# Kernel optimization log

Hardware: AMD Instinct MI355X
Metric: run time of the kernel (lower is better)

Reference implementation:

```python
import jax, jax.numpy as jnp
import numpy as np

D = 1024      # model_dim
H = 2048      # expert hidden_dim
E = 8         # num routed experts
S = 1         # num shared experts
M = 4         # num modes (1 shared expert per mode)
TOP_K = 2
B, L = 2, 2048


def _ffn(x, w1, b1, w2, b2):
    # x: [T, D]; w1: [..., D, H]; stacked experts via einsum
    h = jnp.einsum('td,edh->teh', x, w1) + b1          # [T, E*, H]
    h = jax.nn.gelu(h)
    return jnp.einsum('teh,ehd->ted', h, w2) + b2      # [T, E*, D]


def setup_inputs() -> dict:
    key = jax.random.key(0)
    ks = jax.random.split(key, 16)
    s = 0.02
    inp = {
        'hidden': jax.random.normal(ks[0], (B, L, D), dtype=jnp.float32),
        'mode_ids': jax.random.randint(ks[1], (B, L), 0, M),
        'router_w': jax.random.normal(ks[2], (D, E), dtype=jnp.float32) * s,
        'router_b': jnp.zeros((E,), dtype=jnp.float32),
        'shared_w1': jax.random.normal(ks[3], (S, D, H), dtype=jnp.float32) * s,
        'shared_b1': jnp.zeros((S, H), dtype=jnp.float32),
        'shared_w2': jax.random.normal(ks[4], (S, H, D), dtype=jnp.float32) * s,
        'shared_b2': jnp.zeros((S, D), dtype=jnp.float32),
        'mode_w1': jax.random.normal(ks[5], (M, D, H), dtype=jnp.float32) * s,
        'mode_b1': jnp.zeros((M, H), dtype=jnp.float32),
        'mode_w2': jax.random.normal(ks[6], (M, H, D), dtype=jnp.float32) * s,
        'mode_b2': jnp.zeros((M, D), dtype=jnp.float32),
        'routed_w1': jax.random.normal(ks[7], (E, D, H), dtype=jnp.float32) * s,
        'routed_b1': jnp.zeros((E, H), dtype=jnp.float32),
        'routed_w2': jax.random.normal(ks[8], (E, H, D), dtype=jnp.float32) * s,
        'routed_b2': jnp.zeros((E, D), dtype=jnp.float32),
    }
    return inp


def reference(hidden, mode_ids, router_w, router_b,
              shared_w1, shared_b1, shared_w2, shared_b2,
              mode_w1, mode_b1, mode_w2, mode_b2,
              routed_w1, routed_b1, routed_w2, routed_b2):
    b, l, d = hidden.shape
    flat = hidden.reshape(b * l, d)                         # [T, D]

    # --- router ---
    router_logits = flat @ router_w + router_b              # [T, E]
    router_probs = jax.nn.softmax(router_logits, axis=-1)
    topk_probs, topk_indices = jax.lax.top_k(router_probs, TOP_K)  # [T, K]

    # --- shared experts (mean over S experts) ---
    shared_out = _ffn(flat, shared_w1, shared_b1, shared_w2, shared_b2).mean(axis=1)  # [T, D]

    # --- mode-conditioned shared experts (1 expert per mode) ---
    mode_flat = mode_ids.reshape(-1)                        # [T]
    mode_onehot = jax.nn.one_hot(mode_flat, M, dtype=flat.dtype)   # [T, M]
    mode_all = _ffn(flat, mode_w1, mode_b1, mode_w2, mode_b2)      # [T, M, D]
    mode_out = jnp.einsum('tm,tmd->td', mode_onehot, mode_all)
    shared_out = shared_out + mode_out

    # --- routed experts: combine weights per (token, expert) ---
    # w[t,e] = sum_k topk_probs[t,k] * (topk_indices[t,k] == e)
    combine_w = jnp.einsum('tke,tk->te',
                           jax.nn.one_hot(topk_indices, E, dtype=flat.dtype),
                           topk_probs)                      # [T, E]
    routed_all = _ffn(flat, routed_w1, routed_b1, routed_w2, routed_b2)  # [T, E, D]
    mixed = jnp.einsum('te,ted->td', combine_w, routed_all)

    output = (shared_out + mixed).reshape(b, l, d)
    aux_logits = router_logits.reshape(b, l, E)
    aux_idx = topk_indices.reshape(b, l, TOP_K)
    aux_probs = topk_probs.reshape(b, l, TOP_K)
    return output, aux_logits, aux_idx, aux_probs
```

## Files before the change

### kernel.cpp

```cpp
#include <hip/hip_runtime.h>
#include <hip/hip_bf16.h>

typedef __hip_bfloat16 bf16t;
using f32x4 = __attribute__((ext_vector_type(4))) float;
using s16x8 = __attribute__((ext_vector_type(8))) short;

#define NTOK 4096
#define DIM 1024
#define HID 2048
#define NEXP 8
#define NMODE 4
#define NGRP 13
#define SLOTS_PAD 16640
#define MAXT 144

static constexpr size_t SZ_WT    = (size_t)NGRP * HID * DIM * 2;
static constexpr size_t OFF_WT1  = 0;
static constexpr size_t OFF_OBUF = 0;
static constexpr size_t OFF_WT2  = OFF_WT1 + SZ_WT;
static constexpr size_t OFF_HBUF = OFF_WT2 + SZ_WT;
static constexpr size_t SZ_HBUF  = (size_t)SLOTS_PAD * HID * 2;
static constexpr size_t OFF_XBF  = OFF_HBUF + SZ_HBUF;
static constexpr size_t SZ_XBF   = (size_t)NTOK * DIM * 2;
static constexpr size_t OFF_B1   = OFF_XBF + SZ_XBF;
static constexpr size_t OFF_B2   = OFF_B1 + (size_t)NGRP * HID * 4;
static constexpr size_t OFF_TP   = OFF_B2 + (size_t)NGRP * DIM * 4;
static constexpr size_t OFF_TI   = OFF_TP + (size_t)NTOK * 2 * 4;
static constexpr size_t OFF_MS   = OFF_TI + (size_t)NTOK * 2 * 4;
static constexpr size_t OFF_R0S  = OFF_MS + (size_t)NTOK * 4;
static constexpr size_t OFF_R1S  = OFF_R0S + (size_t)NTOK * 4;
static constexpr size_t OFF_LIST = OFF_R1S + (size_t)NTOK * 4;
static constexpr size_t OFF_CNT  = OFF_LIST + (size_t)SLOTS_PAD * 4;
static constexpr size_t OFF_CUR  = OFF_CNT + 64;
static constexpr size_t OFF_TC   = OFF_CUR + 64;
static constexpr size_t OFF_TD   = OFF_TC + 16;
static constexpr size_t WS_NEED  = OFF_TD + (size_t)MAXT * 16;

static __device__ __forceinline__ short fb(float f) {
    bf16t h = __float2bfloat16(f);
    short s; __builtin_memcpy(&s, &h, 2); return s;
}
static __device__ __forceinline__ float bf2f(short s) {
    unsigned u = ((unsigned)(unsigned short)s) << 16;
    float f; __builtin_memcpy(&f, &u, 4); return f;
}

static __device__ __forceinline__ float fast_exp(float x) {
#if __has_builtin(__builtin_amdgcn_exp2f)
    return __builtin_amdgcn_exp2f(x * 1.4426950408889634f);
#else
    return exp2f(x * 1.4426950408889634f);
#endif
}
static __device__ __forceinline__ float fast_rcp(float x) {
#if __has_builtin(__builtin_amdgcn_rcpf)
    return __builtin_amdgcn_rcpf(x);
#else
    return 1.0f / x;
#endif
}
static __device__ __forceinline__ float gelu_tanh(float x) {
    float x2 = x * x;
    float u = 0.7978845608028654f * fmaf(0.044715f * x2, x, x);
    u = fminf(u, 15.0f);
    float t = fast_exp(2.0f * u);
    return x * t * fast_rcp(t + 1.0f);
}

typedef __attribute__((address_space(3))) void lds_void;
typedef const __attribute__((address_space(1))) void gbl_void;
static __device__ __forceinline__ void gload16(const void* g, void* l) {
    __builtin_amdgcn_global_load_lds((gbl_void*)g, (lds_void*)l, 16, 0, 0);
}

__global__ void router_k(const float* __restrict__ hidden, const int* __restrict__ mode_ids,
                         const float* __restrict__ rw, const float* __restrict__ rb,
                         float* __restrict__ aux_logits, float* __restrict__ aux_idx,
                         float* __restrict__ aux_probs,
                         float* __restrict__ topk_p, int* __restrict__ topk_i,
                         bf16t* __restrict__ xbf) {
    const int t = blockIdx.x;
    const int lane = threadIdx.x;
    const float* x = hidden + (size_t)t * DIM;
    float acc[NEXP];
#pragma unroll
    for (int e = 0; e < NEXP; e++) acc[e] = 0.f;
#pragma unroll
    for (int i = 0; i < DIM / 64; i++) {
        int d = i * 64 + lane;
        float xv = x[d];
        xbf[(size_t)t * DIM + d] = __float2bfloat16(xv);
        const float4* w = (const float4*)(rw + (size_t)d * NEXP);
        float4 w0 = w[0], w1 = w[1];
        acc[0] += xv * w0.x; acc[1] += xv * w0.y; acc[2] += xv * w0.z; acc[3] += xv * w0.w;
        acc[4] += xv * w1.x; acc[5] += xv * w1.y; acc[6] += xv * w1.z; acc[7] += xv * w1.w;
    }
#pragma unroll
    for (int off = 32; off >= 1; off >>= 1) {
#pragma unroll
        for (int e = 0; e < NEXP; e++) acc[e] += __shfl_down(acc[e], off, 64);
    }
    if (lane == 0) {
        float lg[NEXP], pb[NEXP];
        float mx = -1e30f;
#pragma unroll
        for (int e = 0; e < NEXP; e++) { lg[e] = acc[e] + rb[e]; mx = fmaxf(mx, lg[e]); }
        float s = 0.f;
#pragma unroll
        for (int e = 0; e < NEXP; e++) { pb[e] = expf(lg[e] - mx); s += pb[e]; }
        float inv = 1.f / s;
#pragma unroll
        for (int e = 0; e < NEXP; e++) { pb[e] *= inv; aux_logits[(size_t)t * NEXP + e] = lg[e]; }
        int i1 = 0;
        for (int e = 1; e < NEXP; e++) if (pb[e] > pb[i1]) i1 = e;
        int i2 = (i1 == 0) ? 1 : 0;
        for (int e = 0; e < NEXP; e++) { if (e == i1) continue; if (pb[e] > pb[i2]) i2 = e; }
        aux_idx[t * 2] = (float)i1;  aux_idx[t * 2 + 1] = (float)i2;
        aux_probs[t * 2] = pb[i1];   aux_probs[t * 2 + 1] = pb[i2];
        topk_p[t * 2] = pb[i1];      topk_p[t * 2 + 1] = pb[i2];
        topk_i[t * 2] = i1;          topk_i[t * 2 + 1] = i2;
    }
}

__global__ void count_k(const int* __restrict__ mode_ids, const int* __restrict__ topki,
                        int* __restrict__ cnts) {
    const int lane = threadIdx.x & 63;
    const int wave = threadIdx.x >> 6;
    int local[12];
#pragma unroll
    for (int i = 0; i < 12; i++) local[i] = 0;
    for (int c = wave; c < NTOK / 64; c += 4) {
        const int t = c * 64 + lane;
        const int m  = mode_ids[t];
        const int e0 = topki[t * 2];
        const int e1 = topki[t * 2 + 1];
#pragma unroll
        for (int b = 0; b < 4; b++) {
            unsigned long long k = __ballot(m == b);
            local[b] += __popcll(k);
        }
#pragma unroll
        for (int b = 0; b < 8; b++) {
            local[4 + b] += __popcll(__ballot(e0 == b));
            local[4 + b] += __popcll(__ballot(e1 == b));
        }
    }
    if (lane == 0) {
#pragma unroll
        for (int i = 0; i < 12; i++) atomicAdd(&cnts[i], local[i]);
    }
}

struct TPtr {
    const float* s_w1; const float* s_w2;
    const float* m_w1; const float* m_w2;
    const float* r_w1; const float* r_w2;
};
__global__ void transpose_convert_k(TPtr tp, bf16t* __restrict__ wt1, bf16t* __restrict__ wt2) {
    const size_t MSZ = (size_t)DIM * HID;
    int z = blockIdx.z;
    const float* src; bf16t* dst; int R, C;
    if (z == 0)      { src = tp.s_w1;                    dst = wt1;                 R = DIM; C = HID; }
    else if (z == 1) { src = tp.s_w2;                    dst = wt2;                 R = HID; C = DIM; }
    else if (z < 6)  { int m = z - 2;  src = tp.m_w1 + (size_t)m * MSZ; dst = wt1 + (size_t)(1 + m) * MSZ; R = DIM; C = HID; }
    else if (z < 10) { int m = z - 6;  src = tp.m_w2 + (size_t)m * MSZ; dst = wt2 + (size_t)(1 + m) * MSZ; R = HID; C = DIM; }
    else if (z < 18) { int e = z - 10; src = tp.r_w1 + (size_t)e * MSZ; dst = wt1 + (size_t)(5 + e) * MSZ; R = DIM; C = HID; }
    else             { int e = z - 18; src = tp.r_w2 + (size_t)e * MSZ; dst = wt2 + (size_t)(5 + e) * MSZ; R = HID; C = DIM; }
    int c0 = blockIdx.x * 64, r0 = blockIdx.y * 64;
    if (c0 >= C || r0 >= R) return;
    __shared__ float lds[64][65];
    const int t = threadIdx.x;
    const int ar = t >> 4, ac = (t & 15) * 4;
#pragma unroll
    for (int p = 0; p < 4; p++) {
        const int r = p * 16 + ar;
        const float4 v = *(const float4*)(src + (size_t)(r0 + r) * C + (c0 + ac));
        lds[r][ac] = v.x; lds[r][ac + 1] = v.y; lds[r][ac + 2] = v.z; lds[r][ac + 3] = v.w;
    }
    __syncthreads();
    const int bc = t >> 3;
    const int rg = (t & 7) * 8;
#pragma unroll
    for (int j = 0; j < 2; j++) {
        const int c = j * 32 + bc;
        unsigned w[4];
#pragma unroll
        for (int u = 0; u < 4; u++) {
            unsigned lo = (unsigned short)fb(lds[rg + 2 * u][c]);
            unsigned hi = (unsigned short)fb(lds[rg + 2 * u + 1][c]);
            w[u] = (hi << 16) | lo;
        }
        *(uint4*)((char*)dst + ((size_t)(c0 + c) * R + (r0 + rg)) * 2) = make_uint4(w[0], w[1], w[2], w[3]);
    }
}

__global__ void biascat_k(const float* __restrict__ sb1, const float* __restrict__ mb1, const float* __restrict__ rb1,
                          const float* __restrict__ sb2, const float* __restrict__ mb2, const float* __restrict__ rb2,
                          float* __restrict__ B1c, float* __restrict__ B2c) {
    int i = blockIdx.x * 256 + threadIdx.x;
    if (i < NGRP * HID) {
        int g = i / HID, h = i % HID;
        B1c[i] = (g == 0) ? sb1[h] : (g < 5) ? mb1[(g - 1) * HID + h] : rb1[(g - 5) * HID + h];
    }
    if (i < NGRP * DIM) {
        int g = i / DIM, d = i % DIM;
        B2c[i] = (g == 0) ? sb2[d] : (g < 5) ? mb2[(g - 1) * DIM + d] : rb2[(g - 5) * DIM + d];
    }
}

__global__ void scan_k(const int* __restrict__ cnts, int* __restrict__ cursors,
                       int4* __restrict__ tdesc, int* __restrict__ tcount) {
    if (threadIdx.x != 0 || blockIdx.x != 0) return;
    int nt = 0;
    auto emit = [&](int off, int c, int g) {
        for (int r0 = 0; r0 < c; r0 += 128) tdesc[nt++] = make_int4(off + r0, min(128, c - r0), g, 0);
    };
    emit(0, NTOK, 0);
    int off = NTOK;
    for (int m = 0; m < NMODE; m++) { cursors[m] = off; emit(off, cnts[m], 1 + m); off += cnts[m]; }
    off = 2 * NTOK;
    for (int e = 0; e < NEXP; e++) { cursors[NMODE + e] = off; emit(off, cnts[NMODE + e], 5 + e); off += cnts[NMODE + e]; }
    tcount[0] = nt;
}

__global__ void fill_k(const int* __restrict__ mode_ids, const int* __restrict__ topk_i,
                       int* __restrict__ cursors, int* __restrict__ list,
                       int* __restrict__ ms, int* __restrict__ r0s, int* __restrict__ r1s) {
    const int t = blockIdx.x * 256 + threadIdx.x;
    const int lane = threadIdx.x & 63;
    list[t] = t << 1;
    const int m  = mode_ids[t];
    const int e0 = topk_i[t * 2], e1 = topk_i[t * 2 + 1];

    auto put = [&](int bin, bool pred, int payload, int* inv) {
        unsigned long long msk = __ballot(pred);
        if (msk == 0ull) return;
        int leader = __ffsll((unsigned long long)msk) - 1;
        int base = 0;
        if (lane == leader) base = atomicAdd(&cursors[bin], __popcll(msk));
        base = __shfl(base, leader, 64);
        if (pred) {
            int pos = base + __popcll(msk & ((1ull << lane) - 1ull));
            list[pos] = payload;
            inv[t] = pos;
        }
    };
#pragma unroll
    for (int b = 0; b < NMODE; b++) put(b, m == b, t << 1, ms);
#pragma unroll
    for (int b = 0; b < NEXP; b++) put(NMODE + b, e0 == b, t << 1, r0s);
#pragma unroll
    for (int b = 0; b < NEXP; b++) put(NMODE + b, e1 == b, (t << 1) | 1, r1s);
}

template <int STAGE>
__global__ __launch_bounds__(256, 3) void ffn_gemm_k(
    const bf16t* __restrict__ xbf,
    const bf16t* __restrict__ hbuf,
    const bf16t* __restrict__ wt,
    const float* __restrict__ bias,
    bf16t* __restrict__ obuf,
    const int* __restrict__ list,
    const int4* __restrict__ tdesc,
    const int* __restrict__ tcount) {
    constexpr int K   = (STAGE == 1) ? DIM : HID;
    constexpr int N   = (STAGE == 1) ? HID : DIM;
    constexpr int NK  = K / 32;
    constexpr int NTN = N / 128;
    constexpr int NWG = NTN * MAXT;

    const int lin = blockIdx.x;
    const int wg  = (lin & 7) * (NWG >> 3) + (lin >> 3);
    const int ntile = wg / MAXT;
    const int tix = wg - ntile * MAXT;
    if (tix >= tcount[0]) return;
    const int4 td = tdesc[tix];
    const int slot0 = td.x, rows = td.y, gidx = td.z;
    const int n0 = ntile * 128;

    __shared__ alignas(16) char As[3 * 8192];
    __shared__ alignas(16) char Bs[3 * 8192];

    const int tid  = threadIdx.x;
    const int lane = tid & 63;
    const int w    = tid >> 6;
    const int wm   = w >> 1, wn = w & 1;

    const bf16t* wbase = wt + (size_t)gidx * ((size_t)K * N);
    const bf16t* aP[2];
    const bf16t* bP[2];
#pragma unroll
    for (int h = 0; h < 2; h++) {
        const int r  = (w * 2 + h) * 16 + (lane >> 2);
        const int ce = (((lane & 3) ^ ((r >> 1) & 3)) << 3);
        if (STAGE == 1) aP[h] = xbf + (size_t)(list[slot0 + r] >> 1) * DIM + ce;
        else            aP[h] = hbuf + (size_t)(slot0 + r) * HID + ce;
        bP[h] = wbase + (size_t)(n0 + r) * K + ce;
    }

    auto stage = [&](int t) {
        char* la = As + (t % 3) * 8192 + (w * 2) * 1024 + lane * 16;
        char* lb = Bs + (t % 3) * 8192 + (w * 2) * 1024 + lane * 16;
        gload16(aP[0] + t * 32, la);
        gload16(aP[1] + t * 32, la + 1024);
        gload16(bP[0] + t * 32, lb);
        gload16(bP[1] + t * 32, lb + 1024);
    };

    f32x4 acc[4][4];
    const f32x4 zero = {0.f, 0.f, 0.f, 0.f};
#pragma unroll
    for (int i = 0; i < 4; i++)
#pragma unroll
        for (int j = 0; j < 4; j++) acc[i][j] = zero;

    const int lm = lane & 15;
    const int kc = lane >> 4;

    stage(0); stage(1);

    for (int t = 0; t < NK; ++t) {
        const int cur = t % 3;
        if (t + 1 < NK) asm volatile("s_waitcnt vmcnt(4)" ::: "memory");
        else            asm volatile("s_waitcnt vmcnt(0)" ::: "memory");
        __builtin_amdgcn_s_barrier();

        s16x8 av[4], bv[4];
#pragma unroll
        for (int i = 0; i < 4; i++) {
            const int Ra = wm * 64 + i * 16 + lm;
            av[i] = *(const s16x8*)(As + cur * 8192 + Ra * 64 + ((kc ^ ((Ra >> 1) & 3)) << 4));
            const int Rb = wn * 64 + i * 16 + lm;
            bv[i] = *(const s16x8*)(Bs + cur * 8192 + Rb * 64 + ((kc ^ ((Rb >> 1) & 3)) << 4));
        }
        if (t + 2 < NK) stage(t + 2);

        __builtin_amdgcn_s_setprio(1);
#pragma unroll
        for (int mi = 0; mi < 4; mi++)
#pragma unroll
            for (int ni = 0; ni < 4; ni++)
                acc[mi][ni] = __builtin_amdgcn_mfma_f32_16x16x32_bf16(av[mi], bv[ni], acc[mi][ni], 0, 0, 0);
        __builtin_amdgcn_s_setprio(0);
    }

    const int lr = lane >> 4, lc = lane & 15;
#pragma unroll
    for (int ni = 0; ni < 4; ni++) {
        const int col = n0 + wn * 64 + ni * 16 + lc;
        const float bvv = bias[gidx * N + col];
#pragma unroll
        for (int mi = 0; mi < 4; mi++) {
#pragma unroll
            for (int r = 0; r < 4; r++) {
                const int row = wm * 64 + mi * 16 + lr * 4 + r;
                if (row < rows) {
                    float v = acc[mi][ni][r] + bvv;
                    if (STAGE == 1) v = gelu_tanh(v);
                    obuf[(size_t)(slot0 + row) * N + col] = __float2bfloat16(v);
                }
            }
        }
    }
}

__global__ void reduce_k(const bf16t* __restrict__ ob,
                         const int* __restrict__ ms, const int* __restrict__ r0s, const int* __restrict__ r1s,
                         const float* __restrict__ topkp, float* __restrict__ out) {
    const int t = blockIdx.x;
    const int d = threadIdx.x * 8;
    const s16x8 a = *(const s16x8*)(ob + (size_t)t * DIM + d);
    const s16x8 b = *(const s16x8*)(ob + (size_t)ms[t] * DIM + d);
    const s16x8 c = *(const s16x8*)(ob + (size_t)r0s[t] * DIM + d);
    const s16x8 e = *(const s16x8*)(ob + (size_t)r1s[t] * DIM + d);
    const float p0 = topkp[t * 2], p1 = topkp[t * 2 + 1];
    float o[8];
#pragma unroll
    for (int j = 0; j < 8; j++)
        o[j] = bf2f(a[j]) + bf2f(b[j]) + p0 * bf2f(c[j]) + p1 * bf2f(e[j]);
    float* dst = out + (size_t)t * DIM + d;
    *(float4*)dst = make_float4(o[0], o[1], o[2], o[3]);
    *(float4*)(dst + 4) = make_float4(o[4], o[5], o[6], o[7]);
}

extern "C" void kernel_launch(void* const* d_in, const int* in_sizes, int n_in,
                              void* d_out, int out_size, void* d_ws, size_t ws_size,
                              hipStream_t stream) {
    (void)in_sizes; (void)n_in; (void)out_size;
    if (ws_size < WS_NEED) return;

    const float* hidden   = (const float*)d_in[0];
    const int*   mode_ids = (const int*)d_in[1];
    const float* router_w = (const float*)d_in[2];
    const float* router_b = (const float*)d_in[3];
    TPtr tp;
    tp.s_w1 = (const float*)d_in[4];
    const float* s_b1 = (const float*)d_in[5];
    tp.s_w2 = (const float*)d_in[6];
    const float* s_b2 = (const float*)d_in[7];
    tp.m_w1 = (const float*)d_in[8];
    const float* m_b1 = (const float*)d_in[9];
    tp.m_w2 = (const float*)d_in[10];
    const float* m_b2 = (const float*)d_in[11];
    tp.r_w1 = (const float*)d_in[12];
    const float* r_b1 = (const float*)d_in[13];
    tp.r_w2 = (const float*)d_in[14];
    const float* r_b2 = (const float*)d_in[15];

    char* ws = (char*)d_ws;
    bf16t* WT1   = (bf16t*)(ws + OFF_WT1);
    bf16t* WT2   = (bf16t*)(ws + OFF_WT2);
    bf16t* Hbuf  = (bf16t*)(ws + OFF_HBUF);
    bf16t* Xbf   = (bf16t*)(ws + OFF_XBF);
    bf16t* Obuf  = (bf16t*)(ws + OFF_OBUF);
    float* B1c   = (float*)(ws + OFF_B1);
    float* B2c   = (float*)(ws + OFF_B2);
    float* topkp = (float*)(ws + OFF_TP);
    int*   topki = (int*)(ws + OFF_TI);
    int*   ms    = (int*)(ws + OFF_MS);
    int*   r0s   = (int*)(ws + OFF_R0S);
    int*   r1s   = (int*)(ws + OFF_R1S);
    int*   list  = (int*)(ws + OFF_LIST);
    int*   cnts  = (int*)(ws + OFF_CNT);
    int*   curs  = (int*)(ws + OFF_CUR);
    int*   tcnt  = (int*)(ws + OFF_TC);
    int4*  td    = (int4*)(ws + OFF_TD);

    float* out        = (float*)d_out;
    float* aux_logits = out + (size_t)NTOK * DIM;
    float* aux_idx    = aux_logits + (size_t)NTOK * NEXP;
    float* aux_probs  = aux_idx + (size_t)NTOK * 2;

    hipMemsetAsync(ws + OFF_LIST, 0, OFF_TC - OFF_LIST, stream);

    transpose_convert_k<<<dim3(32, 32, 26), 256, 0, stream>>>(tp, WT1, WT2);
    biascat_k<<<(NGRP * HID + 255) / 256, 256, 0, stream>>>(s_b1, m_b1, r_b1, s_b2, m_b2, r_b2, B1c, B2c);
    router_k<<<NTOK, 64, 0, stream>>>(hidden, mode_ids, router_w, router_b,
                                      aux_logits, aux_idx, aux_probs, topkp, topki, Xbf);
    count_k<<<1, 256, 0, stream>>>(mode_ids, topki, cnts);
    scan_k<<<1, 64, 0, stream>>>(cnts, curs, td, tcnt);
    fill_k<<<NTOK / 256, 256, 0, stream>>>(mode_ids, topki, curs, list, ms, r0s, r1s);
    ffn_gemm_k<1><<<(HID / 128) * MAXT, 256, 0, stream>>>(Xbf, Hbuf, WT1, B1c, Hbuf, list, td, tcnt);
    ffn_gemm_k<2><<<(DIM / 128) * MAXT, 256, 0, stream>>>(Xbf, Hbuf, WT2, B2c, Obuf, list, td, tcnt);
    reduce_k<<<NTOK, 128, 0, stream>>>(Obuf, ms, r0s, r1s, topkp, out);
}
```

Baseline: 381.1 us.

## Batch tokens per block, parallelize count, and issue GEMM prefetch earlier

Several independent tweaks. router_k and reduce_k now handle four tokens per block, and count_k runs on 8 blocks instead of 1. Each transpose block now converts two row tiles. In the FFN GEMM, the stage-(t+2) prefetch is issued right after the barrier instead of after the LDS fragment reads, with rotating buffer indices replacing modulo. The aim is to cut launch and tail overhead in the small kernels and to overlap global-to-LDS loads with compute; the risk is that prefetching into the buffer read two iterations ago must not race with other waves still reading it.

```diff
diff --git a/kernel.cpp b/kernel.cpp
--- a/kernel.cpp
+++ b/kernel.cpp
@@ -79,8 +79,8 @@
                          float* __restrict__ aux_probs,
                          float* __restrict__ topk_p, int* __restrict__ topk_i,
                          bf16t* __restrict__ xbf) {
-    const int t = blockIdx.x;
-    const int lane = threadIdx.x;
+    const int t = blockIdx.x * 4 + (threadIdx.x >> 6);
+    const int lane = threadIdx.x & 63;
     const float* x = hidden + (size_t)t * DIM;
     float acc[NEXP];
 #pragma unroll
@@ -129,16 +129,13 @@
     int local[12];
 #pragma unroll
     for (int i = 0; i < 12; i++) local[i] = 0;
-    for (int c = wave; c < NTOK / 64; c += 4) {
+    for (int c = blockIdx.x * 4 + wave; c < NTOK / 64; c += 32) {
         const int t = c * 64 + lane;
         const int m  = mode_ids[t];
         const int e0 = topki[t * 2];
         const int e1 = topki[t * 2 + 1];
 #pragma unroll
-        for (int b = 0; b < 4; b++) {
-            unsigned long long k = __ballot(m == b);
-            local[b] += __popcll(k);
-        }
+        for (int b = 0; b < 4; b++) local[b] += __popcll(__ballot(m == b));
 #pragma unroll
         for (int b = 0; b < 8; b++) {
             local[4 + b] += __popcll(__ballot(e0 == b));
@@ -166,31 +163,37 @@
     else if (z < 10) { int m = z - 6;  src = tp.m_w2 + (size_t)m * MSZ; dst = wt2 + (size_t)(1 + m) * MSZ; R = HID; C = DIM; }
     else if (z < 18) { int e = z - 10; src = tp.r_w1 + (size_t)e * MSZ; dst = wt1 + (size_t)(5 + e) * MSZ; R = DIM; C = HID; }
     else             { int e = z - 18; src = tp.r_w2 + (size_t)e * MSZ; dst = wt2 + (size_t)(5 + e) * MSZ; R = HID; C = DIM; }
-    int c0 = blockIdx.x * 64, r0 = blockIdx.y * 64;
-    if (c0 >= C || r0 >= R) return;
+    const int c0 = blockIdx.x * 64;
+    if (c0 >= C) return;
     __shared__ float lds[64][65];
     const int t = threadIdx.x;
     const int ar = t >> 4, ac = (t & 15) * 4;
-#pragma unroll
-    for (int p = 0; p < 4; p++) {
-        const int r = p * 16 + ar;
-        const float4 v = *(const float4*)(src + (size_t)(r0 + r) * C + (c0 + ac));
-        lds[r][ac] = v.x; lds[r][ac + 1] = v.y; lds[r][ac + 2] = v.z; lds[r][ac + 3] = v.w;
-    }
-    __syncthreads();
     const int bc = t >> 3;
     const int rg = (t & 7) * 8;
 #pragma unroll
-    for (int j = 0; j < 2; j++) {
-        const int c = j * 32 + bc;
-        unsigned w[4];
-#pragma unroll
-        for (int u = 0; u < 4; u++) {
-            unsigned lo = (unsigned short)fb(lds[rg + 2 * u][c]);
-            unsigned hi = (unsigned short)fb(lds[rg + 2 * u + 1][c]);
-            w[u] = (hi << 16) | lo;
-        }
-        *(uint4*)((char*)dst + ((size_t)(c0 + c) * R + (r0 + rg)) * 2) = make_uint4(w[0], w[1], w[2], w[3]);
+    for (int it = 0; it < 2; ++it) {
+        const int r0 = (blockIdx.y * 2 + it) * 64;
+        if (r0 >= R) break;
+#pragma unroll
+        for (int p = 0; p < 4; p++) {
+            const int r = p * 16 + ar;
+            const float4 v = *(const float4*)(src + (size_t)(r0 + r) * C + (c0 + ac));
+            lds[r][ac] = v.x; lds[r][ac + 1] = v.y; lds[r][ac + 2] = v.z; lds[r][ac + 3] = v.w;
+        }
+        __syncthreads();
+#pragma unroll
+        for (int j = 0; j < 2; j++) {
+            const int c = j * 32 + bc;
+            unsigned w[4];
+#pragma unroll
+            for (int u = 0; u < 4; u++) {
+                unsigned lo = (unsigned short)fb(lds[rg + 2 * u][c]);
+                unsigned hi = (unsigned short)fb(lds[rg + 2 * u + 1][c]);
+                w[u] = (hi << 16) | lo;
+            }
+            *(uint4*)((char*)dst + ((size_t)(c0 + c) * R + (r0 + rg)) * 2) = make_uint4(w[0], w[1], w[2], w[3]);
+        }
+        __syncthreads();
     }
 }
 
@@ -298,9 +301,9 @@
         bP[h] = wbase + (size_t)(n0 + r) * K + ce;
     }
 
-    auto stage = [&](int t) {
-        char* la = As + (t % 3) * 8192 + (w * 2) * 1024 + lane * 16;
-        char* lb = Bs + (t % 3) * 8192 + (w * 2) * 1024 + lane * 16;
+    auto stage = [&](int t, int buf) {
+        char* la = As + buf * 8192 + (w * 2) * 1024 + lane * 16;
+        char* lb = Bs + buf * 8192 + (w * 2) * 1024 + lane * 16;
         gload16(aP[0] + t * 32, la);
         gload16(aP[1] + t * 32, la + 1024);
         gload16(bP[0] + t * 32, lb);
@@ -317,13 +320,15 @@
     const int lm = lane & 15;
     const int kc = lane >> 4;
 
-    stage(0); stage(1);
-
+    stage(0, 0); stage(1, 1);
+
+    int cur = 0, pfb = 2;
     for (int t = 0; t < NK; ++t) {
-        const int cur = t % 3;
         if (t + 1 < NK) asm volatile("s_waitcnt vmcnt(4)" ::: "memory");
         else            asm volatile("s_waitcnt vmcnt(0)" ::: "memory");
         __builtin_amdgcn_s_barrier();
+
+        if (t + 2 < NK) stage(t + 2, pfb);
 
         s16x8 av[4], bv[4];
 #pragma unroll
@@ -333,7 +338,6 @@
             const int Rb = wn * 64 + i * 16 + lm;
             bv[i] = *(const s16x8*)(Bs + cur * 8192 + Rb * 64 + ((kc ^ ((Rb >> 1) & 3)) << 4));
         }
-        if (t + 2 < NK) stage(t + 2);
 
         __builtin_amdgcn_s_setprio(1);
 #pragma unroll
@@ -342,6 +346,9 @@
             for (int ni = 0; ni < 4; ni++)
                 acc[mi][ni] = __builtin_amdgcn_mfma_f32_16x16x32_bf16(av[mi], bv[ni], acc[mi][ni], 0, 0, 0);
         __builtin_amdgcn_s_setprio(0);
+
+        cur = (cur == 2) ? 0 : cur + 1;
+        pfb = (pfb == 2) ? 0 : pfb + 1;
     }
 
     const int lr = lane >> 4, lc = lane & 15;
@@ -367,8 +374,8 @@
 __global__ void reduce_k(const bf16t* __restrict__ ob,
                          const int* __restrict__ ms, const int* __restrict__ r0s, const int* __restrict__ r1s,
                          const float* __restrict__ topkp, float* __restrict__ out) {
-    const int t = blockIdx.x;
-    const int d = threadIdx.x * 8;
+    const int t = blockIdx.x * 4 + (threadIdx.x >> 7);
+    const int d = (threadIdx.x & 127) * 8;
     const s16x8 a = *(const s16x8*)(ob + (size_t)t * DIM + d);
     const s16x8 b = *(const s16x8*)(ob + (size_t)ms[t] * DIM + d);
     const s16x8 c = *(const s16x8*)(ob + (size_t)r0s[t] * DIM + d);
@@ -433,14 +440,14 @@
 
     hipMemsetAsync(ws + OFF_LIST, 0, OFF_TC - OFF_LIST, stream);
 
-    transpose_convert_k<<<dim3(32, 32, 26), 256, 0, stream>>>(tp, WT1, WT2);
+    transpose_convert_k<<<dim3(32, 16, 26), 256, 0, stream>>>(tp, WT1, WT2);
     biascat_k<<<(NGRP * HID + 255) / 256, 256, 0, stream>>>(s_b1, m_b1, r_b1, s_b2, m_b2, r_b2, B1c, B2c);
-    router_k<<<NTOK, 64, 0, stream>>>(hidden, mode_ids, router_w, router_b,
-                                      aux_logits, aux_idx, aux_probs, topkp, topki, Xbf);
-    count_k<<<1, 256, 0, stream>>>(mode_ids, topki, cnts);
+    router_k<<<NTOK / 4, 256, 0, stream>>>(hidden, mode_ids, router_w, router_b,
+                                           aux_logits, aux_idx, aux_probs, topkp, topki, Xbf);
+    count_k<<<8, 256, 0, stream>>>(mode_ids, topki, cnts);
     scan_k<<<1, 64, 0, stream>>>(cnts, curs, td, tcnt);
     fill_k<<<NTOK / 256, 256, 0, stream>>>(mode_ids, topki, curs, list, ms, r0s, r1s);
     ffn_gemm_k<1><<<(HID / 128) * MAXT, 256, 0, stream>>>(Xbf, Hbuf, WT1, B1c, Hbuf, list, td, tcnt);
     ffn_gemm_k<2><<<(DIM / 128) * MAXT, 256, 0, stream>>>(Xbf, Hbuf, WT2, B2c, Obuf, list, td, tcnt);
-    reduce_k<<<NTOK, 128, 0, stream>>>(Obuf, ms, r0s, r1s, topkp, out);
-}
+    reduce_k<<<NTOK / 4, 512, 0, stream>>>(Obuf, ms, r0s, r1s, topkp, out);
+}
```

After: 387.2 us. Within noise of the previous version (+1.6%).
